# Performance work log

Hardware: AMD Instinct MI355X
Metric: run time of the kernel (lower is better)

The kernel has to match this reference:

```python
import jax, jax.numpy as jnp
import numpy as np

MARGIN = 0.5
EPSILON = 0.1
LAMBDA_ORDER = 1.0
LAMBDA_CAUSALITY = 0.8
LAMBDA_TRANSITIVITY = 0.6
LOG_CLAMP = -100.0  # torch BCELoss clamps log outputs at -100


def setup_inputs() -> dict:
    key = jax.random.key(0)
    k1, k2, k3, k4, k5 = jax.random.split(key, 5)
    B, S = 4, 2048
    pred_times = jax.random.normal(k1, (B, S), dtype=jnp.float32)
    pred_causal = jax.random.uniform(k2, (B, S, S), dtype=jnp.float32)
    target_times = jax.random.normal(k3, (B, S), dtype=jnp.float32)
    target_causal = jax.random.randint(k4, (B, S, S), 0, 2).astype(jnp.int32)
    target_precedence = jax.random.randint(k5, (B, S, S), 0, 2).astype(jnp.int32)
    return {
        'pred_times': pred_times,
        'pred_causal': pred_causal,
        'target_times': target_times,
        'target_causal': target_causal,
        'target_precedence': target_precedence,
    }


def reference(pred_times, pred_causal, target_times, target_causal, target_precedence):
    B, S = pred_times.shape

    # --- ordering loss ---
    # time_diff[b,i,j] = pred_times[b,i] - pred_times[b,j]
    time_diff = pred_times[:, :, None] - pred_times[:, None, :]
    target_order = (target_times[:, :, None] < target_times[:, None, :]).astype(pred_times.dtype)
    ordering_loss = jnp.mean(jax.nn.relu(MARGIN - time_diff * target_order))

    # --- causality loss (BCE, matching torch.nn.BCELoss log clamping) ---
    t = target_causal.astype(pred_causal.dtype)
    log_p = jnp.maximum(jnp.log(pred_causal), LOG_CLAMP)
    log_1mp = jnp.maximum(jnp.log1p(-pred_causal), LOG_CLAMP)
    causality_loss = -jnp.mean(t * log_p + (1.0 - t) * log_1mp)

    # --- transitivity loss ---
    # Original triple loop: for i<j<k, if precedence[0,i,k]>0 add
    # mean_b relu(eps - (pt[:,k]-pt[:,i])). The body depends only on (i,k);
    # j contributes multiplicity (k-i-1). Collapse to a weighted pair sum.
    idx = jnp.arange(S)
    gap = idx[None, :] - idx[:, None]              # k - i
    mult = jnp.where(gap >= 2, gap - 1, 0).astype(pred_times.dtype)  # (k-i-1) for k>=i+2
    w = mult * (target_precedence[0] > 0).astype(pred_times.dtype)   # [S,S]
    # violation[b,i,k] = relu(eps - (pred_times[b,k] - pred_times[b,i]))
    violation = jax.nn.relu(EPSILON - (pred_times[:, None, :] - pred_times[:, :, None]))
    trans_sum = jnp.sum(w * jnp.mean(violation, axis=0))
    denom = max(1, S * (S - 1) * (S - 2) / 6)
    transitivity_loss = trans_sum / jnp.asarray(denom, dtype=pred_times.dtype)

    total_loss = (LAMBDA_ORDER * ordering_loss
                  + LAMBDA_CAUSALITY * causality_loss
                  + LAMBDA_TRANSITIVITY * transitivity_loss)
    return ordering_loss, causality_loss, transitivity_loss, total_loss
```

## Files before the change

### kernel.cpp

```cpp
#include <hip/hip_runtime.h>

#define S 2048
#define BB 4
#define BLOCK 256
#define NB 8192
#define NTHREADS (NB * BLOCK)
#define NQ_BCE (BB * S * S / 4)
#define TR_PER_BLOCK 128

__global__ __launch_bounds__(BLOCK, 4) void tcl_main(
    const float* __restrict__ pred_times,
    const float* __restrict__ pred_causal,
    const float* __restrict__ target_times,
    const int*   __restrict__ target_causal,
    const int*   __restrict__ target_prec,
    float* __restrict__ partials)
{
    const int t   = threadIdx.x;
    const int bid = blockIdx.x;

    int4 prec = make_int4(0, 0, 0, 0);
    int i = 0, j0 = 0;
    const bool do_tr = (t < TR_PER_BLOCK);
    if (do_tr) {
        const int qt = bid * TR_PER_BLOCK + t;
        i  = qt >> 9;
        j0 = (qt & 511) << 2;
        prec = *(const int4*)(target_prec + (size_t)i * S + j0);
    }
    const size_t g = (size_t)bid * BLOCK + t;
    const float4 pc0 = *(const float4*)(pred_causal + 4 * g);
    const int4   tc0 = *(const int4*)(target_causal + 4 * g);
    const float4 pc1 = *(const float4*)(pred_causal + 4 * (g + (size_t)NTHREADS));
    const int4   tc1 = *(const int4*)(target_causal + 4 * (g + (size_t)NTHREADS));

    float ord = 0.f, trans = 0.f;

    if (do_tr) {
        const int pv[4] = {prec.x, prec.y, prec.z, prec.w};
        float w[4];
#pragma unroll
        for (int l = 0; l < 4; ++l) {
            const int gap = (j0 + l) - i;
            w[l] = (pv[l] > 0 && gap >= 2) ? (float)(gap - 1) : 0.f;
        }
#pragma unroll
        for (int b = 0; b < BB; ++b) {
            const float  pti = pred_times[b * S + i];
            const float  tti = target_times[b * S + i];
            const float4 ptj = *(const float4*)(pred_times + b * S + j0);
            const float4 ttj = *(const float4*)(target_times + b * S + j0);
            const float ptjl[4] = {ptj.x, ptj.y, ptj.z, ptj.w};
            const float ttjl[4] = {ttj.x, ttj.y, ttj.z, ttj.w};
#pragma unroll
            for (int l = 0; l < 4; ++l) {
                const float diff = pti - ptjl[l];
                ord   += (tti < ttjl[l]) ? fmaxf(0.5f - diff, 0.f) : 0.5f;
                trans += w[l] * fmaxf(0.1f + diff, 0.f);
            }
        }
    }

    const float pcl[8] = {pc0.x, pc0.y, pc0.z, pc0.w, pc1.x, pc1.y, pc1.z, pc1.w};
    const int   tcl[8] = {tc0.x, tc0.y, tc0.z, tc0.w, tc1.x, tc1.y, tc1.z, tc1.w};
    float x[8];
#pragma unroll
    for (int l = 0; l < 8; ++l) {
        const float v = (tcl[l] != 0) ? pcl[l] : (1.f - pcl[l]);
        x[l] = fmaxf(v, 1e-9f);
    }
    const float pA = x[0] * x[1], pB = x[2] * x[3], pC = x[4] * x[5], pD = x[6] * x[7];
    float bce = -__logf((pA * pB) * (pC * pD));

#pragma unroll
    for (int off = 32; off > 0; off >>= 1) {
        ord   += __shfl_down(ord, off);
        bce   += __shfl_down(bce, off);
        trans += __shfl_down(trans, off);
    }
    __shared__ float s_o[BLOCK / 64], s_c[BLOCK / 64], s_t[BLOCK / 64];
    const int lane = t & 63;
    const int wv   = t >> 6;
    if (lane == 0) { s_o[wv] = ord; s_c[wv] = bce; s_t[wv] = trans; }
    __syncthreads();
    if (t == 0) {
        float o = 0.f, c = 0.f, tr = 0.f;
#pragma unroll
        for (int k = 0; k < BLOCK / 64; ++k) { o += s_o[k]; c += s_c[k]; tr += s_t[k]; }
        partials[bid]          = o;
        partials[NB + bid]     = c;
        partials[2 * NB + bid] = tr;
    }
}

#define BLOCK_F 1024

__global__ __launch_bounds__(BLOCK_F) void tcl_finalize(
    const float* __restrict__ partials, float* __restrict__ out)
{
    const int t = threadIdx.x;
    float o = 0.f, c = 0.f, tr = 0.f;
#pragma unroll
    for (int it = 0; it < NB / BLOCK_F; ++it) {
        const int k = t + it * BLOCK_F;
        o  += partials[k];
        c  += partials[NB + k];
        tr += partials[2 * NB + k];
    }
#pragma unroll
    for (int off = 32; off > 0; off >>= 1) {
        o  += __shfl_down(o, off);
        c  += __shfl_down(c, off);
        tr += __shfl_down(tr, off);
    }
    __shared__ float s_o[BLOCK_F / 64], s_c[BLOCK_F / 64], s_t[BLOCK_F / 64];
    const int lane = t & 63;
    const int wv   = t >> 6;
    if (lane == 0) { s_o[wv] = o; s_c[wv] = c; s_t[wv] = tr; }
    __syncthreads();
    if (t == 0) {
        float so = 0.f, sc = 0.f, st = 0.f;
#pragma unroll
        for (int k = 0; k < BLOCK_F / 64; ++k) { so += s_o[k]; sc += s_c[k]; st += s_t[k]; }
        const double cnt   = (double)BB * S * S;
        const double denom = 2048.0 * 2047.0 * 2046.0 / 6.0;
        const float ordm = (float)((double)so / cnt);
        const float bcem = (float)((double)sc / cnt);
        const float trm  = (float)((double)st / (double)BB / denom);
        out[0] = ordm;
        out[1] = bcem;
        out[2] = trm;
        out[3] = 1.0f * ordm + 0.8f * bcem + 0.6f * trm;
    }
}

extern "C" void kernel_launch(void* const* d_in, const int* in_sizes, int n_in,
                              void* d_out, int out_size, void* d_ws, size_t ws_size,
                              hipStream_t stream) {
    const float* pred_times    = (const float*)d_in[0];
    const float* pred_causal   = (const float*)d_in[1];
    const float* target_times  = (const float*)d_in[2];
    const int*   target_causal = (const int*)d_in[3];
    const int*   target_prec   = (const int*)d_in[4];
    float* out      = (float*)d_out;
    float* partials = (float*)d_ws;

    tcl_main<<<dim3(NB), dim3(BLOCK), 0, stream>>>(
        pred_times, pred_causal, target_times, target_causal, target_prec, partials);
    tcl_finalize<<<dim3(1), dim3(BLOCK_F), 0, stream>>>(partials, out);
}
```

Baseline: 187.0 us.

## Use persistent-style grid with software-pipelined nontemporal loads for BCE

Cuts the grid from 8192 to 2048 blocks, so each thread now handles 8 BCE float4 chunks and 2 transitivity/ordering quads instead of 2 and one half-occupied quad. The BCE loop keeps two loads in flight ahead of the compute, a register-level software pipeline, and all streaming loads use nontemporal hints to avoid cache pollution. Launch bounds are raised to 8 blocks per CU. This aims to reduce block launch and reduction overhead and improve memory-level parallelism. It changes the probability clamp from 1e-9 to 1e-8, which slightly alters numerics, and it adds register pressure.

```diff
diff --git a/kernel.cpp b/kernel.cpp
--- a/kernel.cpp
+++ b/kernel.cpp
@@ -3,12 +3,22 @@
 #define S 2048
 #define BB 4
 #define BLOCK 256
-#define NB 8192
-#define NTHREADS (NB * BLOCK)
-#define NQ_BCE (BB * S * S / 4)
-#define TR_PER_BLOCK 128
+#define NB 2048
+#define NT (NB * BLOCK)
+#define BCE_IT 8
+#define TR_IT 2
 
-__global__ __launch_bounds__(BLOCK, 4) void tcl_main(
+typedef float fx4 __attribute__((ext_vector_type(4)));
+typedef int   ix4 __attribute__((ext_vector_type(4)));
+
+__device__ __forceinline__ fx4 ntld4f(const float* p) {
+    return __builtin_nontemporal_load((const fx4*)p);
+}
+__device__ __forceinline__ ix4 ntld4i(const int* p) {
+    return __builtin_nontemporal_load((const ix4*)p);
+}
+
+__global__ __launch_bounds__(BLOCK, 8) void tcl_main(
     const float* __restrict__ pred_times,
     const float* __restrict__ pred_causal,
     const float* __restrict__ target_times,
@@ -18,31 +28,33 @@
 {
     const int t   = threadIdx.x;
     const int bid = blockIdx.x;
+    const size_t g0 = (size_t)bid * BLOCK + t;
 
-    int4 prec = make_int4(0, 0, 0, 0);
-    int i = 0, j0 = 0;
-    const bool do_tr = (t < TR_PER_BLOCK);
-    if (do_tr) {
-        const int qt = bid * TR_PER_BLOCK + t;
-        i  = qt >> 9;
-        j0 = (qt & 511) << 2;
-        prec = *(const int4*)(target_prec + (size_t)i * S + j0);
+    fx4 pcA = ntld4f(pred_causal + 4 * g0);
+    ix4 tcA = ntld4i(target_causal + 4 * g0);
+    fx4 pcB = ntld4f(pred_causal + 4 * (g0 + (size_t)NT));
+    ix4 tcB = ntld4i(target_causal + 4 * (g0 + (size_t)NT));
+
+    ix4 prec[TR_IT];
+    int ti[TR_IT], tj[TR_IT];
+#pragma unroll
+    for (int n = 0; n < TR_IT; ++n) {
+        const int qt = (int)(g0 + (size_t)n * NT);
+        ti[n] = qt >> 9;
+        tj[n] = (qt & 511) << 2;
+        prec[n] = ntld4i(target_prec + (size_t)ti[n] * S + tj[n]);
     }
-    const size_t g = (size_t)bid * BLOCK + t;
-    const float4 pc0 = *(const float4*)(pred_causal + 4 * g);
-    const int4   tc0 = *(const int4*)(target_causal + 4 * g);
-    const float4 pc1 = *(const float4*)(pred_causal + 4 * (g + (size_t)NTHREADS));
-    const int4   tc1 = *(const int4*)(target_causal + 4 * (g + (size_t)NTHREADS));
 
-    float ord = 0.f, trans = 0.f;
+    float ord = 0.f, bce = 0.f, trans = 0.f;
 
-    if (do_tr) {
-        const int pv[4] = {prec.x, prec.y, prec.z, prec.w};
+#pragma unroll
+    for (int n = 0; n < TR_IT; ++n) {
+        const int i = ti[n], j0 = tj[n];
         float w[4];
 #pragma unroll
         for (int l = 0; l < 4; ++l) {
             const int gap = (j0 + l) - i;
-            w[l] = (pv[l] > 0 && gap >= 2) ? (float)(gap - 1) : 0.f;
+            w[l] = (prec[n][l] > 0 && gap >= 2) ? (float)(gap - 1) : 0.f;
         }
 #pragma unroll
         for (int b = 0; b < BB; ++b) {
@@ -61,16 +73,24 @@
         }
     }
 
-    const float pcl[8] = {pc0.x, pc0.y, pc0.z, pc0.w, pc1.x, pc1.y, pc1.z, pc1.w};
-    const int   tcl[8] = {tc0.x, tc0.y, tc0.z, tc0.w, tc1.x, tc1.y, tc1.z, tc1.w};
-    float x[8];
 #pragma unroll
-    for (int l = 0; l < 8; ++l) {
-        const float v = (tcl[l] != 0) ? pcl[l] : (1.f - pcl[l]);
-        x[l] = fmaxf(v, 1e-9f);
+    for (int it = 0; it < BCE_IT; ++it) {
+        fx4 pcN = pcB; ix4 tcN = tcB;
+        if (it + 2 < BCE_IT) {
+            const size_t g = g0 + (size_t)(it + 2) * NT;
+            pcN = ntld4f(pred_causal + 4 * g);
+            tcN = ntld4i(target_causal + 4 * g);
+        }
+        float x[4];
+#pragma unroll
+        for (int l = 0; l < 4; ++l) {
+            const float v = (tcA[l] != 0) ? pcA[l] : (1.f - pcA[l]);
+            x[l] = fmaxf(v, 1e-8f);
+        }
+        bce -= __logf((x[0] * x[1]) * (x[2] * x[3]));
+        pcA = pcB; tcA = tcB;
+        pcB = pcN; tcB = tcN;
     }
-    const float pA = x[0] * x[1], pB = x[2] * x[3], pC = x[4] * x[5], pD = x[6] * x[7];
-    float bce = -__logf((pA * pB) * (pC * pD));
 
 #pragma unroll
     for (int off = 32; off > 0; off >>= 1) {
```

Result: faster. 177.8 us (median of 2 runs) (-5.0%).
